# Performance work log

Hardware: AMD Instinct MI355X
Metric: run time of the kernel (lower is better)

Reference implementation:

```python
import jax, jax.numpy as jnp
import numpy as np

B, C_LEN, Q_LEN, D = 8, 2048, 512, 1024


def setup_inputs() -> dict:
    key = jax.random.key(0)
    ks = jax.random.split(key, 10)
    scale = 1.0 / np.sqrt(D)
    return {
        "c": jax.random.normal(ks[0], (B, C_LEN, D), dtype=jnp.float32),
        "q": jax.random.normal(ks[1], (B, Q_LEN, D), dtype=jnp.float32),
        "w_cq": jax.random.normal(ks[2], (D,), dtype=jnp.float32) * scale,
        "b_cq": jax.random.normal(ks[3], (), dtype=jnp.float32) * scale,
        "w_c": jax.random.normal(ks[4], (D,), dtype=jnp.float32) * scale,
        "b_c": jax.random.normal(ks[5], (), dtype=jnp.float32) * scale,
        "w_q": jax.random.normal(ks[6], (D,), dtype=jnp.float32) * scale,
        "b_q": jax.random.normal(ks[7], (), dtype=jnp.float32) * scale,
        "W_l": jax.random.normal(ks[8], (D, 4 * D), dtype=jnp.float32) * (1.0 / np.sqrt(4 * D)),
        "b_l": jax.random.normal(ks[9], (D,), dtype=jnp.float32) * (1.0 / np.sqrt(4 * D)),
    }


def reference(c, q, w_cq, b_cq, w_c, b_c, w_q, b_q, W_l, b_l):
    # trilinear term: the original loops over q positions computing
    # att_weight_cq(c * q_i); since that Linear is rank-1, this is one einsum.
    cq = jnp.einsum('bcd,bqd,d->bcq', c, q, w_cq) + b_cq        # [B, C, Q]
    s = (c @ w_c + b_c)[:, :, None] + (q @ w_q + b_q)[:, None, :] + cq
    a = jax.nn.softmax(s, axis=2)                               # c2q attention
    c2q_att = jnp.einsum('bcq,bqd->bcd', a, q)                  # [B, C, D]
    b_att = jax.nn.softmax(jnp.max(s, axis=2), axis=1)          # [B, C]
    q2c_att = jnp.einsum('bc,bcd->bd', b_att, c)[:, None, :]    # [B, 1, D]
    x = jnp.concatenate([c, c2q_att, c * c2q_att, c * q2c_att], axis=-1)
    z = x @ W_l.T + b_l                                         # [B, C, D]
    return z
```

## Files before the change

### kernel.cpp

```cpp
#include <hip/hip_runtime.h>

typedef unsigned short u16;
typedef __attribute__((ext_vector_type(4))) float floatx4;
typedef __attribute__((ext_vector_type(4))) unsigned short u16x4;
typedef __attribute__((ext_vector_type(8))) short short8;
typedef __attribute__((ext_vector_type(8))) __bf16 bf16x8;

#define B_SZ 8
#define C_LEN 2048
#define Q_LEN 512
#define D_DIM 1024
#define K4 (4 * D_DIM)

static __device__ __forceinline__ u16 f2bf(float f) {
    union { float f; unsigned int u; } v; v.f = f;
    unsigned int r = v.u + 0x7FFFu + ((v.u >> 16) & 1u);
    return (u16)(r >> 16);
}
static __device__ __forceinline__ float bf2f(u16 h) {
    union { unsigned int u; float f; } v; v.u = ((unsigned int)h) << 16;
    return v.f;
}

static __device__ __forceinline__ void async16(const void* g, void* l) {
    __builtin_amdgcn_global_load_lds(
        (const __attribute__((address_space(1))) unsigned int*)g,
        (__attribute__((address_space(3))) unsigned int*)(unsigned int)(unsigned long long)l,
        16, 0, 0);
}

__global__ __launch_bounds__(256) void precast_c(const float* __restrict__ c, const float* __restrict__ w_c,
                                                 u16* __restrict__ cbf, float* __restrict__ rowterm) {
    int row = blockIdx.x * 4 + (threadIdx.x >> 6);
    int lane = threadIdx.x & 63;
    const float* src = c + (size_t)row * D_DIM;
    u16* dst = cbf + (size_t)row * D_DIM;
    float s = 0.f;
    #pragma unroll
    for (int j = 0; j < 4; ++j) {
        int idx = j * 256 + lane * 4;
        floatx4 a = *(const floatx4*)(src + idx);
        floatx4 w = *(const floatx4*)(w_c + idx);
        s += a[0]*w[0] + a[1]*w[1] + a[2]*w[2] + a[3]*w[3];
        u16x4 o;
        #pragma unroll
        for (int e = 0; e < 4; ++e) o[e] = f2bf(a[e]);
        *(u16x4*)(dst + idx) = o;
    }
    for (int off = 32; off; off >>= 1) s += __shfl_down(s, off);
    if (lane == 0) rowterm[row] = s;
}

__global__ __launch_bounds__(256) void precast_q(const float* __restrict__ q, const float* __restrict__ w_cq,
                                                 const float* __restrict__ w_q,
                                                 u16* __restrict__ qwbf, float* __restrict__ colterm) {
    int row = blockIdx.x * 4 + (threadIdx.x >> 6);
    int lane = threadIdx.x & 63;
    const float* src = q + (size_t)row * D_DIM;
    u16* dst = qwbf + (size_t)row * D_DIM;
    float s = 0.f;
    #pragma unroll
    for (int j = 0; j < 4; ++j) {
        int idx = j * 256 + lane * 4;
        floatx4 a  = *(const floatx4*)(src + idx);
        floatx4 wc = *(const floatx4*)(w_cq + idx);
        floatx4 wq = *(const floatx4*)(w_q + idx);
        s += a[0]*wq[0] + a[1]*wq[1] + a[2]*wq[2] + a[3]*wq[3];
        u16x4 o;
        #pragma unroll
        for (int e = 0; e < 4; ++e) o[e] = f2bf(a[e] * wc[e]);
        *(u16x4*)(dst + idx) = o;
    }
    for (int off = 32; off; off >>= 1) s += __shfl_down(s, off);
    if (lane == 0) colterm[row] = s;
}

__global__ __launch_bounds__(256) void precast_W(const float* __restrict__ W, u16* __restrict__ Wbf) {
    int t = blockIdx.x * 256 + threadIdx.x;
    int e4 = t * 4;
    int n = e4 >> 11;
    int kk = e4 & 2047;
    floatx4 v = *(const floatx4*)(W + (size_t)n * K4 + 1024 + kk);
    u16x4 o;
    #pragma unroll
    for (int e = 0; e < 4; ++e) o[e] = f2bf(v[e]);
    *(u16x4*)(Wbf + (size_t)n * 2048 + kk) = o;
}

__global__ void transpose_q_kernel(const float* __restrict__ q, u16* __restrict__ qT) {
    __shared__ float tile[32][33];
    int b = blockIdx.z;
    int q0 = blockIdx.x * 32;
    int d0 = blockIdx.y * 32;
    int tx = threadIdx.x, ty = threadIdx.y;
    const float* qb = q + (size_t)b * Q_LEN * D_DIM;
    #pragma unroll
    for (int j = 0; j < 4; ++j) {
        int row = ty + j * 8;
        tile[row][tx] = qb[(size_t)(q0 + row) * D_DIM + d0 + tx];
    }
    __syncthreads();
    u16* qTb = qT + (size_t)b * D_DIM * Q_LEN;
    #pragma unroll
    for (int j = 0; j < 4; ++j) {
        int row = ty + j * 8;
        qTb[(size_t)(d0 + row) * Q_LEN + q0 + tx] = f2bf(tile[tx][row]);
    }
}

template<int MODE>
__global__ __launch_bounds__(256) void gemm_async(
    const u16* __restrict__ A0, const u16* __restrict__ A1, const u16* __restrict__ A2,
    const u16* __restrict__ B0, const u16* __restrict__ B1,
    float* __restrict__ of, u16* __restrict__ ob, const float* __restrict__ bias) {
    constexpr int NSEC = (MODE == 2) ? 3 : 1;
    constexpr int KSEC = (MODE == 1) ? 512 : 1024;
    constexpr int LDO  = (MODE == 0) ? 512 : 1024;
    __shared__ u16 As[128 * 64];
    __shared__ u16 Bs[128 * 64];
    const int tid  = threadIdx.x;
    const int lane = tid & 63;
    const int wave = tid >> 6;
    const int b    = blockIdx.z;
    const int n0   = blockIdx.x * 128;
    const int m0   = blockIdx.y * 128;

    const u16* Aarr[NSEC];
    const u16* Barr[NSEC];
    int lda_[NSEC], ldb_[NSEC];
    if constexpr (MODE == 0) {
        Aarr[0] = A0 + (size_t)b * C_LEN * D_DIM; lda_[0] = 1024;
        Barr[0] = B0 + (size_t)b * Q_LEN * D_DIM; ldb_[0] = 1024;
    } else if constexpr (MODE == 1) {
        Aarr[0] = A0 + (size_t)b * C_LEN * Q_LEN; lda_[0] = 512;
        Barr[0] = B0 + (size_t)b * D_DIM * Q_LEN; ldb_[0] = 512;
    } else {
        Aarr[0] = A0 + (size_t)b * C_LEN * D_DIM;  lda_[0] = 1024;
        Barr[0] = B0 + (size_t)b * D_DIM * D_DIM;  ldb_[0] = 1024;
        Aarr[1] = A1 + (size_t)b * C_LEN * 2048;        lda_[1] = 2048;
        Barr[1] = B1;                                   ldb_[1] = 2048;
        Aarr[2] = A1 + (size_t)b * C_LEN * 2048 + 1024; lda_[2] = 2048;
        Barr[2] = B1 + 1024;                            ldb_[2] = 2048;
    }

    const int srow = lane >> 3;
    const int ssc  = ((lane & 7) ^ srow) * 8;

    floatx4 acc[4][4];
    #pragma unroll
    for (int i = 0; i < 4; ++i)
        #pragma unroll
        for (int j = 0; j < 4; ++j)
            acc[i][j] = (floatx4)(0.0f);

    const int wrow = (wave >> 1) * 64;
    const int wcol = (wave & 1) * 64;
    const int quad = lane >> 4;
    const int lrow = lane & 15;
    const int sw7  = lane & 7;

    #pragma unroll
    for (int sec = 0; sec < NSEC; ++sec) {
        const u16* __restrict__ Ab = Aarr[sec];
        const u16* __restrict__ Bb = Barr[sec];
        const int LA = lda_[sec];
        const int LB = ldb_[sec];
        for (int k0 = 0; k0 < KSEC; k0 += 64) {
            #pragma unroll
            for (int cc = 0; cc < 4; ++cc) {
                int ch = wave * 4 + cc;
                int rr = ch * 8 + srow;
                async16(Ab + (size_t)(m0 + rr) * LA + k0 + ssc, &As[ch * 512]);
            }
            #pragma unroll
            for (int cc = 0; cc < 4; ++cc) {
                int ch = wave * 4 + cc;
                int rr = ch * 8 + srow;
                async16(Bb + (size_t)(n0 + rr) * LB + k0 + ssc, &Bs[ch * 512]);
            }
            __syncthreads();
            #pragma unroll
            for (int h = 0; h < 2; ++h) {
                const int pc = ((h * 4 + quad) ^ sw7) * 8;
                bf16x8 af[4], bfr[4];
                #pragma unroll
                for (int i = 0; i < 4; ++i)
                    af[i] = __builtin_bit_cast(bf16x8, *(const short8*)&As[(wrow + i*16 + lrow) * 64 + pc]);
                #pragma unroll
                for (int j = 0; j < 4; ++j)
                    bfr[j] = __builtin_bit_cast(bf16x8, *(const short8*)&Bs[(wcol + j*16 + lrow) * 64 + pc]);
                #pragma unroll
                for (int i = 0; i < 4; ++i)
                    #pragma unroll
                    for (int j = 0; j < 4; ++j)
                        acc[i][j] = __builtin_amdgcn_mfma_f32_16x16x32_bf16(af[i], bfr[j], acc[i][j], 0, 0, 0);
            }
            __syncthreads();
        }
    }

    float* ofb = nullptr; u16* ccb = nullptr; const u16* cbr = nullptr;
    if (MODE == 0)      ofb = of + (size_t)b * C_LEN * Q_LEN;
    else if (MODE == 1) { ccb = ob + (size_t)b * C_LEN * 2048; cbr = A1 + (size_t)b * C_LEN * D_DIM; }
    else                ofb = of + (size_t)b * C_LEN * D_DIM;
    #pragma unroll
    for (int i = 0; i < 4; ++i) {
        #pragma unroll
        for (int j = 0; j < 4; ++j) {
            #pragma unroll
            for (int e = 0; e < 4; ++e) {
                int gm = m0 + wrow + i * 16 + quad * 4 + e;
                int gn = n0 + wcol + j * 16 + lrow;
                float v = acc[i][j][e];
                if (MODE == 0)      ofb[(size_t)gm * LDO + gn] = v;
                else if (MODE == 1) {
                    u16 p = f2bf(v);
                    float cv = bf2f(cbr[(size_t)gm * 1024 + gn]);
                    ccb[(size_t)gm * 2048 + gn]        = p;
                    ccb[(size_t)gm * 2048 + 1024 + gn] = f2bf(cv * bf2f(p));
                }
                else                ofb[(size_t)gm * LDO + gn] = v + bias[gn];
            }
        }
    }
}

__global__ void softmax_kernel(const float* __restrict__ S, const float* __restrict__ colterm,
                               u16* __restrict__ P, float* __restrict__ mbuf) {
    int row = blockIdx.x * 4 + (threadIdx.x >> 6);
    int lane = threadIdx.x & 63;
    int b = row >> 11;
    const float* sp = S + (size_t)row * Q_LEN;
    const float* cp = colterm + (size_t)b * Q_LEN;
    float v[8];
    float m = -1e30f;
    #pragma unroll
    for (int j = 0; j < 8; ++j) {
        int idx = j * 64 + lane;
        v[j] = sp[idx] + cp[idx];
        m = fmaxf(m, v[j]);
    }
    for (int off = 32; off; off >>= 1) m = fmaxf(m, __shfl_xor(m, off));
    float s = 0.f;
    #pragma unroll
    for (int j = 0; j < 8; ++j) { v[j] = __expf(v[j] - m); s += v[j]; }
    for (int off = 32; off; off >>= 1) s += __shfl_xor(s, off);
    float inv = 1.0f / s;
    u16* pp = P + (size_t)row * Q_LEN;
    #pragma unroll
    for (int j = 0; j < 8; ++j) pp[j * 64 + lane] = f2bf(v[j] * inv);
    if (lane == 0) mbuf[row] = m;
}

__global__ __launch_bounds__(256) void batt_kernel(const float* __restrict__ mbuf,
                                                   const float* __restrict__ rowterm,
                                                   float* __restrict__ batt) {
    __shared__ float red[8];
    int b = blockIdx.x;
    int tid = threadIdx.x;
    const float* mb = mbuf + (size_t)b * C_LEN;
    const float* rt = rowterm + (size_t)b * C_LEN;
    float v[8];
    float m = -1e30f;
    #pragma unroll
    for (int j = 0; j < 8; ++j) { int idx = j * 256 + tid; v[j] = mb[idx] + rt[idx]; m = fmaxf(m, v[j]); }
    for (int off = 32; off; off >>= 1) m = fmaxf(m, __shfl_xor(m, off));
    int wave = tid >> 6, lane = tid & 63;
    if (lane == 0) red[wave] = m;
    __syncthreads();
    m = fmaxf(fmaxf(red[0], red[1]), fmaxf(red[2], red[3]));
    float s = 0.f;
    #pragma unroll
    for (int j = 0; j < 8; ++j) { v[j] = __expf(v[j] - m); s += v[j]; }
    for (int off = 32; off; off >>= 1) s += __shfl_xor(s, off);
    if (lane == 0) red[4 + wave] = s;
    __syncthreads();
    s = red[4] + red[5] + red[6] + red[7];
    float inv = 1.0f / s;
    float* bb = batt + (size_t)b * C_LEN;
    #pragma unroll
    for (int j = 0; j < 8; ++j) bb[j * 256 + tid] = v[j] * inv;
}

__global__ __launch_bounds__(256) void q2c_kernel(const float* __restrict__ batt,
                                                  const u16* __restrict__ cbf,
                                                  float* __restrict__ q2c) {
    int d  = blockIdx.x * 256 + threadIdx.x;
    int b  = blockIdx.y;
    int c0 = blockIdx.z * 256;
    const u16* cb = cbf + ((size_t)b * C_LEN + c0) * D_DIM + d;
    const float* bb = batt + (size_t)b * C_LEN + c0;
    float s = 0.f;
    #pragma unroll 4
    for (int i = 0; i < 256; ++i) s += bb[i] * bf2f(cb[(size_t)i * D_DIM]);
    atomicAdd(&q2c[(size_t)b * D_DIM + d], s);
}

__global__ __launch_bounds__(256) void wmerge_kernel(const float* __restrict__ W, const float* __restrict__ q2c,
                                                     u16* __restrict__ Wm) {
    int b = blockIdx.y;
    int i = (blockIdx.x * 256 + threadIdx.x) * 4;
    int n = i >> 10, k = i & 1023;
    floatx4 w1 = *(const floatx4*)(W + (size_t)n * K4 + k);
    floatx4 w4 = *(const floatx4*)(W + (size_t)n * K4 + 3072 + k);
    floatx4 g  = *(const floatx4*)(q2c + (size_t)b * D_DIM + k);
    u16x4 o;
    #pragma unroll
    for (int e = 0; e < 4; ++e) o[e] = f2bf(w1[e] + w4[e] * g[e]);
    *(u16x4*)(Wm + (size_t)b * 1048576 + i) = o;
}

extern "C" void kernel_launch(void* const* d_in, const int* in_sizes, int n_in,
                              void* d_out, int out_size, void* d_ws, size_t ws_size,
                              hipStream_t stream) {
    const float* c   = (const float*)d_in[0];
    const float* q   = (const float*)d_in[1];
    const float* wcq = (const float*)d_in[2];
    const float* w_c = (const float*)d_in[4];
    const float* w_q = (const float*)d_in[6];
    const float* W_l = (const float*)d_in[8];
    const float* b_l = (const float*)d_in[9];
    float* out = (float*)d_out;

    char* ws = (char*)d_ws;
    u16*   cbf     = (u16*)ws;
    float* S       = (float*)(ws + 33554432);
    u16*   CC      = (u16*)(ws + 33554432);
    u16*   qwbf    = (u16*)(ws + 67108864);
    u16*   P       = (u16*)(ws + 100663296);
    u16*   Wm      = (u16*)(ws + 100663296);
    u16*   qT      = (u16*)(ws + 117440512);
    u16*   Wbf     = (u16*)(ws + 117440512);
    float* rowterm = (float*)(ws + 125829120);
    float* colterm = (float*)(ws + 125894656);
    float* mbuf    = (float*)(ws + 125911040);
    float* batt    = (float*)(ws + 125976576);
    float* q2c     = (float*)(ws + 126042112);

    hipMemsetAsync(q2c, 0, B_SZ * D_DIM * sizeof(float), stream);
    precast_c<<<dim3(4096), dim3(256), 0, stream>>>(c, w_c, cbf, rowterm);
    precast_q<<<dim3(1024), dim3(256), 0, stream>>>(q, wcq, w_q, qwbf, colterm);
    transpose_q_kernel<<<dim3(16, 32, 8), dim3(32, 8), 0, stream>>>(q, qT);
    gemm_async<0><<<dim3(4, 16, 8), dim3(256), 0, stream>>>(cbf, nullptr, nullptr, qwbf, nullptr, S, nullptr, nullptr);
    softmax_kernel<<<dim3(4096), dim3(256), 0, stream>>>(S, colterm, P, mbuf);
    batt_kernel<<<dim3(8), dim3(256), 0, stream>>>(mbuf, rowterm, batt);
    q2c_kernel<<<dim3(4, 8, 8), dim3(256), 0, stream>>>(batt, cbf, q2c);
    gemm_async<1><<<dim3(8, 16, 8), dim3(256), 0, stream>>>(P, cbf, nullptr, qT, nullptr, nullptr, CC, nullptr);
    wmerge_kernel<<<dim3(1024, 8), dim3(256), 0, stream>>>(W_l, q2c, Wm);
    precast_W<<<dim3(2048), dim3(256), 0, stream>>>(W_l, Wbf);
    gemm_async<2><<<dim3(8, 16, 8), dim3(256), 0, stream>>>(cbf, CC, nullptr, Wm, Wbf, out, nullptr, b_l);
}
```

Before: 397.1 us.

## Fuse prep kernels, merge W casts, and remap GEMM grids batch-innermost

```diff
diff --git a/kernel.cpp b/kernel.cpp
--- a/kernel.cpp
+++ b/kernel.cpp
@@ -29,82 +29,101 @@
         16, 0, 0);
 }
 
-__global__ __launch_bounds__(256) void precast_c(const float* __restrict__ c, const float* __restrict__ w_c,
-                                                 u16* __restrict__ cbf, float* __restrict__ rowterm) {
-    int row = blockIdx.x * 4 + (threadIdx.x >> 6);
-    int lane = threadIdx.x & 63;
-    const float* src = c + (size_t)row * D_DIM;
-    u16* dst = cbf + (size_t)row * D_DIM;
-    float s = 0.f;
-    #pragma unroll
-    for (int j = 0; j < 4; ++j) {
-        int idx = j * 256 + lane * 4;
-        floatx4 a = *(const floatx4*)(src + idx);
-        floatx4 w = *(const floatx4*)(w_c + idx);
-        s += a[0]*w[0] + a[1]*w[1] + a[2]*w[2] + a[3]*w[3];
+__global__ __launch_bounds__(256) void prep_kernel(
+    const float* __restrict__ c, const float* __restrict__ q,
+    const float* __restrict__ w_cq, const float* __restrict__ w_c, const float* __restrict__ w_q,
+    u16* __restrict__ cbf, u16* __restrict__ qwbf, u16* __restrict__ qT,
+    float* __restrict__ rowterm, float* __restrict__ colterm, float* __restrict__ q2c) {
+    int blk = blockIdx.x;
+    int tid = threadIdx.x;
+    if (blk < 4096) {
+        int row = blk * 4 + (tid >> 6);
+        int lane = tid & 63;
+        const float* src = c + (size_t)row * D_DIM;
+        u16* dst = cbf + (size_t)row * D_DIM;
+        float s = 0.f;
+        #pragma unroll
+        for (int j = 0; j < 4; ++j) {
+            int idx = j * 256 + lane * 4;
+            floatx4 a = *(const floatx4*)(src + idx);
+            floatx4 w = *(const floatx4*)(w_c + idx);
+            s += a[0]*w[0] + a[1]*w[1] + a[2]*w[2] + a[3]*w[3];
+            u16x4 o;
+            #pragma unroll
+            for (int e = 0; e < 4; ++e) o[e] = f2bf(a[e]);
+            *(u16x4*)(dst + idx) = o;
+        }
+        for (int off = 32; off; off >>= 1) s += __shfl_down(s, off);
+        if (lane == 0) rowterm[row] = s;
+    } else if (blk < 5120) {
+        int row = (blk - 4096) * 4 + (tid >> 6);
+        int lane = tid & 63;
+        const float* src = q + (size_t)row * D_DIM;
+        u16* dst = qwbf + (size_t)row * D_DIM;
+        float s = 0.f;
+        #pragma unroll
+        for (int j = 0; j < 4; ++j) {
+            int idx = j * 256 + lane * 4;
+            floatx4 a  = *(const floatx4*)(src + idx);
+            floatx4 wc = *(const floatx4*)(w_cq + idx);
+            floatx4 wq = *(const floatx4*)(w_q + idx);
+            s += a[0]*wq[0] + a[1]*wq[1] + a[2]*wq[2] + a[3]*wq[3];
+            u16x4 o;
+            #pragma unroll
+            for (int e = 0; e < 4; ++e) o[e] = f2bf(a[e] * wc[e]);
+            *(u16x4*)(dst + idx) = o;
+        }
+        for (int off = 32; off; off >>= 1) s += __shfl_down(s, off);
+        if (lane == 0) colterm[row] = s;
+    } else if (blk < 9216) {
+        __shared__ float tile[32][33];
+        int t = blk - 5120;
+        int q0 = (t & 15) * 32;
+        int d0 = ((t >> 4) & 31) * 32;
+        int b = t >> 9;
+        int tx = tid & 31, ty = tid >> 5;
+        const float* qb = q + (size_t)b * Q_LEN * D_DIM;
+        #pragma unroll
+        for (int j = 0; j < 4; ++j) {
+            int row = ty + j * 8;
+            tile[row][tx] = qb[(size_t)(q0 + row) * D_DIM + d0 + tx];
+        }
+        __syncthreads();
+        u16* qTb = qT + (size_t)b * D_DIM * Q_LEN;
+        #pragma unroll
+        for (int j = 0; j < 4; ++j) {
+            int row = ty + j * 8;
+            qTb[(size_t)(d0 + row) * Q_LEN + q0 + tx] = f2bf(tile[tx][row]);
+        }
+    } else {
+        int i = (blk - 9216) * 256 + tid;
+        q2c[i] = 0.0f;
+    }
+}
+
+__global__ __launch_bounds__(256) void wmerge_all(const float* __restrict__ W, const float* __restrict__ q2c,
+                                                  u16* __restrict__ Wm, u16* __restrict__ Wbf) {
+    int n = blockIdx.x;
+    int k = threadIdx.x * 4;
+    const float* wr = W + (size_t)n * K4;
+    floatx4 w1 = *(const floatx4*)(wr + k);
+    floatx4 w4 = *(const floatx4*)(wr + 3072 + k);
+    #pragma unroll
+    for (int p = 0; p < 2; ++p) {
+        int kk = p * 1024 + k;
+        floatx4 v = *(const floatx4*)(wr + 1024 + kk);
         u16x4 o;
         #pragma unroll
-        for (int e = 0; e < 4; ++e) o[e] = f2bf(a[e]);
-        *(u16x4*)(dst + idx) = o;
-    }
-    for (int off = 32; off; off >>= 1) s += __shfl_down(s, off);
-    if (lane == 0) rowterm[row] = s;
-}
-
-__global__ __launch_bounds__(256) void precast_q(const float* __restrict__ q, const float* __restrict__ w_cq,
-                                                 const float* __restrict__ w_q,
-                                                 u16* __restrict__ qwbf, float* __restrict__ colterm) {
-    int row = blockIdx.x * 4 + (threadIdx.x >> 6);
-    int lane = threadIdx.x & 63;
-    const float* src = q + (size_t)row * D_DIM;
-    u16* dst = qwbf + (size_t)row * D_DIM;
-    float s = 0.f;
-    #pragma unroll
-    for (int j = 0; j < 4; ++j) {
-        int idx = j * 256 + lane * 4;
-        floatx4 a  = *(const floatx4*)(src + idx);
-        floatx4 wc = *(const floatx4*)(w_cq + idx);
-        floatx4 wq = *(const floatx4*)(w_q + idx);
-        s += a[0]*wq[0] + a[1]*wq[1] + a[2]*wq[2] + a[3]*wq[3];
+        for (int e = 0; e < 4; ++e) o[e] = f2bf(v[e]);
+        *(u16x4*)(Wbf + (size_t)n * 2048 + kk) = o;
+    }
+    #pragma unroll
+    for (int b = 0; b < 8; ++b) {
+        floatx4 g = *(const floatx4*)(q2c + (size_t)b * D_DIM + k);
         u16x4 o;
         #pragma unroll
-        for (int e = 0; e < 4; ++e) o[e] = f2bf(a[e] * wc[e]);
-        *(u16x4*)(dst + idx) = o;
-    }
-    for (int off = 32; off; off >>= 1) s += __shfl_down(s, off);
-    if (lane == 0) colterm[row] = s;
-}
-
-__global__ __launch_bounds__(256) void precast_W(const float* __restrict__ W, u16* __restrict__ Wbf) {
-    int t = blockIdx.x * 256 + threadIdx.x;
-    int e4 = t * 4;
-    int n = e4 >> 11;
-    int kk = e4 & 2047;
-    floatx4 v = *(const floatx4*)(W + (size_t)n * K4 + 1024 + kk);
-    u16x4 o;
-    #pragma unroll
-    for (int e = 0; e < 4; ++e) o[e] = f2bf(v[e]);
-    *(u16x4*)(Wbf + (size_t)n * 2048 + kk) = o;
-}
-
-__global__ void transpose_q_kernel(const float* __restrict__ q, u16* __restrict__ qT) {
-    __shared__ float tile[32][33];
-    int b = blockIdx.z;
-    int q0 = blockIdx.x * 32;
-    int d0 = blockIdx.y * 32;
-    int tx = threadIdx.x, ty = threadIdx.y;
-    const float* qb = q + (size_t)b * Q_LEN * D_DIM;
-    #pragma unroll
-    for (int j = 0; j < 4; ++j) {
-        int row = ty + j * 8;
-        tile[row][tx] = qb[(size_t)(q0 + row) * D_DIM + d0 + tx];
-    }
-    __syncthreads();
-    u16* qTb = qT + (size_t)b * D_DIM * Q_LEN;
-    #pragma unroll
-    for (int j = 0; j < 4; ++j) {
-        int row = ty + j * 8;
-        qTb[(size_t)(d0 + row) * Q_LEN + q0 + tx] = f2bf(tile[tx][row]);
+        for (int e = 0; e < 4; ++e) o[e] = f2bf(w1[e] + w4[e] * g[e]);
+        *(u16x4*)(Wm + (size_t)b * 1048576 + (size_t)n * 1024 + k) = o;
     }
 }
 
@@ -116,14 +135,17 @@
     constexpr int NSEC = (MODE == 2) ? 3 : 1;
     constexpr int KSEC = (MODE == 1) ? 512 : 1024;
     constexpr int LDO  = (MODE == 0) ? 512 : 1024;
+    constexpr int NTILES = (MODE == 0) ? 4 : 8;
     __shared__ u16 As[128 * 64];
     __shared__ u16 Bs[128 * 64];
     const int tid  = threadIdx.x;
     const int lane = tid & 63;
     const int wave = tid >> 6;
-    const int b    = blockIdx.z;
-    const int n0   = blockIdx.x * 128;
-    const int m0   = blockIdx.y * 128;
+    const int lin  = blockIdx.x;
+    const int b    = lin & 7;
+    const int rem  = lin >> 3;
+    const int n0   = (rem % NTILES) * 128;
+    const int m0   = (rem / NTILES) * 128;
 
     const u16* Aarr[NSEC];
     const u16* Barr[NSEC];
@@ -296,20 +318,6 @@
     atomicAdd(&q2c[(size_t)b * D_DIM + d], s);
 }
 
-__global__ __launch_bounds__(256) void wmerge_kernel(const float* __restrict__ W, const float* __restrict__ q2c,
-                                                     u16* __restrict__ Wm) {
-    int b = blockIdx.y;
-    int i = (blockIdx.x * 256 + threadIdx.x) * 4;
-    int n = i >> 10, k = i & 1023;
-    floatx4 w1 = *(const floatx4*)(W + (size_t)n * K4 + k);
-    floatx4 w4 = *(const floatx4*)(W + (size_t)n * K4 + 3072 + k);
-    floatx4 g  = *(const floatx4*)(q2c + (size_t)b * D_DIM + k);
-    u16x4 o;
-    #pragma unroll
-    for (int e = 0; e < 4; ++e) o[e] = f2bf(w1[e] + w4[e] * g[e]);
-    *(u16x4*)(Wm + (size_t)b * 1048576 + i) = o;
-}
-
 extern "C" void kernel_launch(void* const* d_in, const int* in_sizes, int n_in,
                               void* d_out, int out_size, void* d_ws, size_t ws_size,
                               hipStream_t stream) {
@@ -337,16 +345,13 @@
     float* batt    = (float*)(ws + 125976576);
     float* q2c     = (float*)(ws + 126042112);
 
-    hipMemsetAsync(q2c, 0, B_SZ * D_DIM * sizeof(float), stream);
-    precast_c<<<dim3(4096), dim3(256), 0, stream>>>(c, w_c, cbf, rowterm);
-    precast_q<<<dim3(1024), dim3(256), 0, stream>>>(q, wcq, w_q, qwbf, colterm);
-    transpose_q_kernel<<<dim3(16, 32, 8), dim3(32, 8), 0, stream>>>(q, qT);
-    gemm_async<0><<<dim3(4, 16, 8), dim3(256), 0, stream>>>(cbf, nullptr, nullptr, qwbf, nullptr, S, nullptr, nullptr);
+    prep_kernel<<<dim3(9248), dim3(256), 0, stream>>>(c, q, wcq, w_c, w_q,
+                                                      cbf, qwbf, qT, rowterm, colterm, q2c);
+    gemm_async<0><<<dim3(512), dim3(256), 0, stream>>>(cbf, nullptr, nullptr, qwbf, nullptr, S, nullptr, nullptr);
     softmax_kernel<<<dim3(4096), dim3(256), 0, stream>>>(S, colterm, P, mbuf);
     batt_kernel<<<dim3(8), dim3(256), 0, stream>>>(mbuf, rowterm, batt);
     q2c_kernel<<<dim3(4, 8, 8), dim3(256), 0, stream>>>(batt, cbf, q2c);
-    gemm_async<1><<<dim3(8, 16, 8), dim3(256), 0, stream>>>(P, cbf, nullptr, qT, nullptr, nullptr, CC, nullptr);
-    wmerge_kernel<<<dim3(1024, 8), dim3(256), 0, stream>>>(W_l, q2c, Wm);
-    precast_W<<<dim3(2048), dim3(256), 0, stream>>>(W_l, Wbf);
-    gemm_async<2><<<dim3(8, 16, 8), dim3(256), 0, stream>>>(cbf, CC, nullptr, Wm, Wbf, out, nullptr, b_l);
-}
+    gemm_async<1><<<dim3(1024), dim3(256), 0, stream>>>(P, cbf, nullptr, qT, nullptr, nullptr, CC, nullptr);
+    wmerge_all<<<dim3(1024), dim3(256), 0, stream>>>(W_l, q2c, Wm, Wbf);
+    gemm_async<2><<<dim3(1024), dim3(256), 0, stream>>>(cbf, CC, nullptr, Wm, Wbf, out, nullptr, b_l);
+}
```

New measurement: 364.8 us. 1.09x faster.
